# Kernel tuning notes

Measured on AMD Instinct MI355X. Metric: run time of the kernel, lower is better.

Reference implementation:

```python
import jax, jax.numpy as jnp
import numpy as np


def setup_inputs() -> dict:
    key = jax.random.key(0)
    ks = jax.random.split(key, 14)
    B, Ld, Lq, D = 64, 512, 128, 512
    d_node = jax.random.normal(ks[0], (B, Ld, D), jnp.float32)
    q_node = jax.random.normal(ks[1], (B, Lq, D), jnp.float32)
    qq_graph = jax.random.randint(ks[2], (B, Lq, Lq), 0, 2, jnp.int32)
    dq_graph = jax.random.randint(ks[3], (B, Ld, Lq), 0, 2, jnp.int32)
    dd_graph = jax.random.randint(ks[4], (B, Ld, Ld), 0, 2, jnp.int32)
    qd_graph = jax.random.randint(ks[5], (B, Lq, Ld), 0, 2, jnp.int32)
    s = 0.02
    W_nw = jax.random.normal(ks[6], (1, D), jnp.float32) * s
    b_nw = jnp.zeros((1,), jnp.float32)
    W_self = jax.random.normal(ks[7], (D, D), jnp.float32) * s
    b_self = jnp.zeros((D,), jnp.float32)
    W_dd = jax.random.normal(ks[8], (D, D), jnp.float32) * s
    W_qq = jax.random.normal(ks[9], (D, D), jnp.float32) * s
    W_dq = jax.random.normal(ks[10], (D, D), jnp.float32) * s
    W_qd = jax.random.normal(ks[11], (D, D), jnp.float32) * s
    return {"d_node": d_node, "q_node": q_node, "qq_graph": qq_graph,
            "dq_graph": dq_graph, "dd_graph": dd_graph, "qd_graph": qd_graph,
            "W_nw": W_nw, "b_nw": b_nw, "W_self": W_self, "b_self": b_self,
            "W_dd": W_dd, "W_qq": W_qq, "W_dq": W_dq, "W_qd": W_qd,
            "iteration_steps": 2}


def reference(d_node, q_node, qq_graph, dq_graph, dd_graph, qd_graph,
              W_nw, b_nw, W_self, b_self, W_dd, W_qq, W_dq, W_qd,
              iteration_steps):
    dd = dd_graph.astype(jnp.float32)
    dq = dq_graph.astype(jnp.float32)
    qq = qq_graph.astype(jnp.float32)
    qd = qd_graph.astype(jnp.float32)

    # neighbor counts, clamped to 1 where a node has no neighbors
    d_nb = dd.sum(-1) + dq.sum(-1)              # [B, Ld]
    d_nb = jnp.where(d_nb >= 1.0, d_nb, 1.0)
    q_nb = qq.sum(-1) + qd.sum(-1)              # [B, Lq]
    q_nb = jnp.where(q_nb >= 1.0, q_nb, 1.0)

    all_d_w, all_q_w = [], []
    for _ in range(iteration_steps):
        d_w = jax.nn.sigmoid(jnp.einsum('bld,od->blo', d_node, W_nw) + b_nw)[..., 0]  # [B, Ld]
        q_w = jax.nn.sigmoid(jnp.einsum('bld,od->blo', q_node, W_nw) + b_nw)[..., 0]  # [B, Lq]
        all_d_w.append(d_w)
        all_q_w.append(q_w)

        self_d = jnp.einsum('bld,od->blo', d_node, W_self) + b_self
        self_q = jnp.einsum('bld,od->blo', q_node, W_self) + b_self
        dd_info = jnp.einsum('bld,od->blo', d_node, W_dd)
        qd_info = jnp.einsum('bld,od->blo', d_node, W_qd)
        qq_info = jnp.einsum('bld,od->blo', q_node, W_qq)
        dq_info = jnp.einsum('bld,od->blo', q_node, W_dq)

        # masked weights: graph is 0/1, so replace_masked_values(., graph, 0) == graph * weight
        dd_msg = jnp.einsum('bij,bjd->bid', dd * d_w[:, None, :], dd_info)  # [B,Ld,D]
        qd_msg = jnp.einsum('bij,bjd->bid', qd * d_w[:, None, :], qd_info)  # [B,Lq,D]
        qq_msg = jnp.einsum('bij,bjd->bid', qq * q_w[:, None, :], qq_info)  # [B,Lq,D]
        dq_msg = jnp.einsum('bij,bjd->bid', dq * q_w[:, None, :], dq_info)  # [B,Ld,D]

        agg_q = (qq_msg + qd_msg) / q_nb[..., None]
        agg_d = (dd_msg + dq_msg) / d_nb[..., None]
        d_node = jax.nn.relu(self_d + agg_d)
        q_node = jax.nn.relu(self_q + agg_q)

    all_d_w = jnp.stack(all_d_w, axis=1)  # [B, steps, Ld]
    all_q_w = jnp.stack(all_q_w, axis=1)  # [B, steps, Lq]
    return (d_node, q_node, all_d_w, all_q_w)
```

## Files before the change

kernel.cpp:

```cpp
#include <hip/hip_runtime.h>
#include <cstdint>
#include <cstddef>

typedef _Float16 h16;
typedef __attribute__((ext_vector_type(8))) _Float16 h16x8;
typedef __attribute__((ext_vector_type(4))) _Float16 h16x4;
typedef __attribute__((ext_vector_type(4))) float f32x4;

constexpr int B_ = 64, LD = 512, LQ = 128, DIM = 512, STEPS = 2;
constexpr int MD = B_ * LD;
constexpr int MQ = B_ * LQ;
constexpr int KST = LD + LQ;
constexpr int KAGG = KST + DIM;

#define ASYNC16(gp, lp)                                                          \
  __builtin_amdgcn_global_load_lds(                                              \
      (const __attribute__((address_space(1))) unsigned int*)(gp),               \
      (__attribute__((address_space(3))) unsigned int*)(lp), 16, 0, 0)

struct Src {
  const h16* p0; int s0; long bstr0;
  const h16* p1; int s1; long bstr1;
  int ksplit;
};

template <int WM, class Epi>
__device__ __forceinline__ void gemm_body(int b, long tileM, long tileN,
                                          Src sa, Src sb, int K,
                                          const Epi& epi, h16* lds) {
  constexpr int BM = WM * 32;
  constexpr int AS = BM / 64;
  constexpr int AE = BM * 32;
  constexpr int BUFE = AE + 4096;

  const int tid = threadIdx.x;
  const int lane = tid & 63;
  const int wv = tid >> 6;
  const int wi = wv >> 1, wj = wv & 1;
  const int quad = lane >> 4, l16 = lane & 15;

  const int r = tid >> 2;
  const int es = (r ^ (r >> 2)) & 3;
  const int kq = (tid & 3) ^ es;

  const h16* pa[2][AS];
  const h16* pb[2][2];
#pragma unroll
  for (int s = 0; s < AS; s++) {
    pa[0][s] = sa.p0 + (size_t)b * sa.bstr0 + (tileM + r + 64 * s) * (long)sa.s0 + kq * 8;
    pa[1][s] = sa.p1 + (size_t)b * sa.bstr1 + (tileM + r + 64 * s) * (long)sa.s1 + kq * 8 - sa.ksplit;
  }
#pragma unroll
  for (int s = 0; s < 2; s++) {
    pb[0][s] = sb.p0 + (size_t)b * sb.bstr0 + (tileN + r + 64 * s) * (long)sb.s0 + kq * 8;
    pb[1][s] = sb.p1 + (size_t)b * sb.bstr1 + (tileN + r + 64 * s) * (long)sb.s1 + kq * 8 - sb.ksplit;
  }

  const int ef = (l16 ^ (l16 >> 2)) & 3;
  int offA[WM], offB[4];
#pragma unroll
  for (int i = 0; i < WM; i++) {
    const int row = wi * WM * 16 + i * 16 + l16;
    offA[i] = (row * 4 + (quad ^ ef)) * 8;
  }
#pragma unroll
  for (int j = 0; j < 4; j++) {
    const int row = wj * 64 + j * 16 + l16;
    offB[j] = AE + (row * 4 + (quad ^ ef)) * 8;
  }

  f32x4 acc[WM][4] = {};
  const int T = K >> 5;

  auto dmaTile = [&](int t, int off) {
    const int k0 = t * 32;
    h16* base = lds + off + tid * 8;
    const int sel = (k0 >= sa.ksplit);
#pragma unroll
    for (int s = 0; s < AS; s++) ASYNC16(pa[sel][s] + k0, base + s * 2048);
    const int selb = (k0 >= sb.ksplit);
#pragma unroll
    for (int s = 0; s < 2; s++) ASYNC16(pb[selb][s] + k0, base + AE + s * 2048);
  };
  auto mfmaStep = [&](int off) {
    h16x8 af[WM], bf[4];
#pragma unroll
    for (int i = 0; i < WM; i++) af[i] = *(const h16x8*)(lds + off + offA[i]);
#pragma unroll
    for (int j = 0; j < 4; j++) bf[j] = *(const h16x8*)(lds + off + offB[j]);
#pragma unroll
    for (int i = 0; i < WM; i++)
#pragma unroll
      for (int j = 0; j < 4; j++)
        acc[i][j] = __builtin_amdgcn_mfma_f32_16x16x32_f16(af[i], bf[j], acc[i][j], 0, 0, 0);
  };

  dmaTile(0, 0);
  dmaTile(1, BUFE);

  int co = 0;
  int no = 2 * BUFE;
  for (int t = 0; t < T - 1; ++t) {
    if constexpr (WM == 8) asm volatile("s_waitcnt vmcnt(6)" ::: "memory");
    else                   asm volatile("s_waitcnt vmcnt(4)" ::: "memory");
    __builtin_amdgcn_s_barrier();
    asm volatile("" ::: "memory");
    __builtin_amdgcn_sched_barrier(0);
    if (t + 2 < T) dmaTile(t + 2, no);
    mfmaStep(co);
    co = (co == 2 * BUFE) ? 0 : co + BUFE;
    no = (no == 2 * BUFE) ? 0 : no + BUFE;
  }
  asm volatile("s_waitcnt vmcnt(0)" ::: "memory");
  __builtin_amdgcn_s_barrier();
  asm volatile("" ::: "memory");
  __builtin_amdgcn_sched_barrier(0);
  mfmaStep(co);

#pragma unroll
  for (int i = 0; i < WM; i++) {
#pragma unroll
    for (int j = 0; j < 4; j++) {
      const int gm0 = (int)tileM + wi * WM * 16 + i * 16 + quad * 4;
      const int gn  = (int)tileN + wj * 64 + j * 16 + l16;
#pragma unroll
      for (int rr = 0; rr < 4; rr++) epi(b, gm0 + rr, gn, acc[i][j][rr]);
    }
  }
}

struct EpiDense {
  const float* w;
  h16* stackA;
  h16* stackB;
  int lnShift;
  int offA, offB;
  __device__ void operator()(int, int gm, int gn, float v) const {
    const int b = gn >> lnShift, l = gn & ((1 << lnShift) - 1);
    const h16 sv = (h16)(w[gn] * v);
    if (gm < 512)
      stackA[((size_t)b * 512 + gm) * 640 + offA + l] = sv;
    else
      stackB[((size_t)b * 512 + (gm - 512)) * 640 + offB + l] = sv;
  }
};
struct EpiAgg {
  const float* bias;
  float* out;
  h16* nodeNext;
  int rowsPerB;
  __device__ void operator()(int b, int gm, int gn, float v) const {
    const size_t row = (size_t)b * rowsPerB + gm;
    const float val = fmaxf(v + bias[gn], 0.f);
    if (out) out[row * 512 + gn] = val;
    if (nodeNext) nodeNext[row * 512 + gn] = (h16)val;
  }
};

__global__ __launch_bounds__(256, 2) void k_dense(Src saD, Src sbD, EpiDense epiD,
                                                  Src saQ, Src sbQ, EpiDense epiQ) {
  __shared__ __align__(16) h16 lds[3 * (256 * 32 + 128 * 32)];
  const int g = blockIdx.x;
  const int x = g / 320;
  const int yy = g % 320;
  if (yy < 256)
    gemm_body<8>(0, (long)x * 256, (long)yy * 128, saD, sbD, 512, epiD, lds);
  else
    gemm_body<8>(0, (long)x * 256, (long)(yy - 256) * 128, saQ, sbQ, 512, epiQ, lds);
}

__global__ __launch_bounds__(256, 2) void k_agg(Src saD, Src sbD, EpiAgg epiD,
                                                Src saQ, Src sbQ, EpiAgg epiQ) {
  __shared__ __align__(16) h16 lds[3 * (256 * 32 + 128 * 32)];
  const int g = blockIdx.x;
  const int b = g & 63;
  const int inner = g >> 6;
  if (inner >= 4) {
    const int i2 = inner - 4;
    gemm_body<8>(b, (long)(i2 >> 2) * 256, (long)(i2 & 3) * 128, saD, sbD, KAGG, epiD, lds);
  } else {
    gemm_body<4>(b, 0L, (long)inner * 128, saQ, sbQ, KAGG, epiQ, lds);
  }
}

__global__ __launch_bounds__(256) void k_convert(const float* __restrict__ dn,
                                                 const float* __restrict__ qn,
                                                 h16* __restrict__ dnb,
                                                 h16* __restrict__ qnb) {
  const size_t i4 = ((size_t)blockIdx.x * 256 + threadIdx.x) * 4;
  constexpr size_t TD = (size_t)MD * DIM;
  const float* src; h16* dst; size_t idx;
  if (i4 < TD) { src = dn; dst = dnb; idx = i4; }
  else         { src = qn; dst = qnb; idx = i4 - TD; }
  const float4 v = *(const float4*)&src[idx];
  h16x4 o; o.x = (h16)v.x; o.y = (h16)v.y; o.z = (h16)v.z; o.w = (h16)v.w;
  *(h16x4*)&dst[idx] = o;
}

__global__ __launch_bounds__(256) void k_wcat(const float* __restrict__ Wself,
                                              const float* __restrict__ Wdd,
                                              const float* __restrict__ Wqd,
                                              const float* __restrict__ Wqq,
                                              const float* __restrict__ Wdq,
                                              h16* __restrict__ catD,
                                              h16* __restrict__ catQ) {
  const int i = blockIdx.x * 256 + threadIdx.x;
  float vD, vQ;
  if (i < 512 * 512)       { vD = Wself[i];            vQ = vD; }
  else if (i < 1024 * 512) { vD = Wdd[i - 512 * 512];  vQ = Wqq[i - 512 * 512]; }
  else                     { vD = Wqd[i - 1024 * 512]; vQ = Wdq[i - 1024 * 512]; }
  catD[i] = (h16)vD; catQ[i] = (h16)vQ;
}

__global__ __launch_bounds__(256) void k_maskD(const int* __restrict__ dd,
                                               const int* __restrict__ dq,
                                               h16* __restrict__ maskD) {
  const int row = blockIdx.x * 4 + (threadIdx.x >> 6);
  const int lane = threadIdx.x & 63;
  const int* pdd = dd + (size_t)row * 512;
  const int* pdq = dq + (size_t)row * 128;
  h16* pm = maskD + (size_t)row * 640;
  float vals[10];
  float s = 0.f;
#pragma unroll
  for (int t = 0; t < 10; t++) {
    const int j = lane + t * 64;
    const float v = (float)((j < 512) ? pdd[j] : pdq[j - 512]);
    vals[t] = v; s += v;
  }
  for (int m = 32; m; m >>= 1) s += __shfl_xor(s, m);
  const float inv = 1.f / fmaxf(s, 1.f);
#pragma unroll
  for (int t = 0; t < 10; t++) pm[lane + t * 64] = (h16)(vals[t] * inv);
}

__global__ __launch_bounds__(256) void k_maskQ(const int* __restrict__ qq,
                                               const int* __restrict__ qd,
                                               h16* __restrict__ maskQ) {
  const int row = blockIdx.x * 4 + (threadIdx.x >> 6);
  const int lane = threadIdx.x & 63;
  const int* pqq = qq + (size_t)row * 128;
  const int* pqd = qd + (size_t)row * 512;
  h16* pm = maskQ + (size_t)row * 640;
  float vals[10];
  float s = 0.f;
#pragma unroll
  for (int t = 0; t < 10; t++) {
    const int j = lane + t * 64;
    const float v = (float)((j < 128) ? pqq[j] : pqd[j - 128]);
    vals[t] = v; s += v;
  }
  for (int m = 32; m; m >>= 1) s += __shfl_xor(s, m);
  const float inv = 1.f / fmaxf(s, 1.f);
#pragma unroll
  for (int t = 0; t < 10; t++) pm[lane + t * 64] = (h16)(vals[t] * inv);
}

__global__ __launch_bounds__(256) void k_w(const h16* __restrict__ dnb,
                                           const h16* __restrict__ qnb,
                                           const float* __restrict__ Wnw,
                                           const float* __restrict__ bnw,
                                           float* __restrict__ d_w,
                                           float* __restrict__ q_w,
                                           float* __restrict__ adw,
                                           float* __restrict__ aqw, int it) {
  const int row = blockIdx.x * 4 + (threadIdx.x >> 6);
  const int lane = threadIdx.x & 63;
  const bool isD = row < MD;
  const h16* node = isD ? dnb + (size_t)row * 512 : qnb + (size_t)(row - MD) * 512;
  const h16x8 v = *(const h16x8*)&node[lane * 8];
  const float4 w0 = *(const float4*)&Wnw[lane * 8];
  const float4 w1 = *(const float4*)&Wnw[lane * 8 + 4];
  float s = (float)v[0] * w0.x + (float)v[1] * w0.y + (float)v[2] * w0.z +
            (float)v[3] * w0.w + (float)v[4] * w1.x + (float)v[5] * w1.y +
            (float)v[6] * w1.z + (float)v[7] * w1.w;
  for (int m = 32; m; m >>= 1) s += __shfl_xor(s, m);
  if (lane == 0) {
    const float w = 1.f / (1.f + expf(-(s + bnw[0])));
    if (isD) {
      d_w[row] = w;
      adw[((size_t)(row >> 9) * STEPS + it) * 512 + (row & 511)] = w;
    } else {
      const int rq = row - MD;
      q_w[rq] = w;
      aqw[((size_t)(rq >> 7) * STEPS + it) * 128 + (rq & 127)] = w;
    }
  }
}

extern "C" void kernel_launch(void* const* d_in, const int* in_sizes, int n_in,
                              void* d_out, int out_size, void* d_ws, size_t ws_size,
                              hipStream_t stream) {
  (void)in_sizes; (void)n_in; (void)out_size; (void)ws_size;

  const float* d_node = (const float*)d_in[0];
  const float* q_node = (const float*)d_in[1];
  const int*   qq     = (const int*)d_in[2];
  const int*   dq     = (const int*)d_in[3];
  const int*   dd     = (const int*)d_in[4];
  const int*   qd     = (const int*)d_in[5];
  const float* W_nw   = (const float*)d_in[6];
  const float* b_nw   = (const float*)d_in[7];
  const float* W_self = (const float*)d_in[8];
  const float* b_self = (const float*)d_in[9];
  const float* W_dd   = (const float*)d_in[10];
  const float* W_qq   = (const float*)d_in[11];
  const float* W_dq   = (const float*)d_in[12];
  const float* W_qd   = (const float*)d_in[13];

  float* outd = (float*)d_out;
  float* outq = outd + (size_t)MD * DIM;
  float* adw  = outq + (size_t)MQ * DIM;
  float* aqw  = adw + (size_t)B_ * STEPS * LD;

  char* p = (char*)d_ws;
  auto alloc = [&](size_t bytes) { char* r = p; p += (bytes + 255) & ~(size_t)255; return r; };
  h16* dnode[2], *qnode[2];
  dnode[0] = (h16*)alloc((size_t)MD * DIM * 2);
  dnode[1] = (h16*)alloc((size_t)MD * DIM * 2);
  qnode[0] = (h16*)alloc((size_t)MQ * DIM * 2);
  qnode[1] = (h16*)alloc((size_t)MQ * DIM * 2);
  h16* catD    = (h16*)alloc((size_t)1536 * 512 * 2);
  h16* catQ    = (h16*)alloc((size_t)1536 * 512 * 2);
  h16* maskD   = (h16*)alloc((size_t)B_ * LD * KST * 2);
  h16* maskQ   = (h16*)alloc((size_t)B_ * LQ * KST * 2);
  h16* stackDT = (h16*)alloc((size_t)B_ * 512 * KST * 2);
  h16* stackQT = (h16*)alloc((size_t)B_ * 512 * KST * 2);
  float* d_wb  = (float*)alloc((size_t)MD * 4);
  float* q_wb  = (float*)alloc((size_t)MQ * 4);

  k_convert<<<dim3((MD * DIM + MQ * DIM) / 4 / 256), 256, 0, stream>>>(d_node, q_node, dnode[0], qnode[0]);
  k_wcat<<<dim3(1536 * 512 / 256), 256, 0, stream>>>(W_self, W_dd, W_qd, W_qq, W_dq, catD, catQ);
  k_maskD<<<dim3(MD / 4), 256, 0, stream>>>(dd, dq, maskD);
  k_maskQ<<<dim3(MQ / 4), 256, 0, stream>>>(qq, qd, maskQ);

  for (int it = 0; it < STEPS; it++) {
    const bool last = (it == STEPS - 1);
    h16* ncur_d = dnode[it & 1];
    h16* nnext_d = dnode[(it & 1) ^ 1];
    h16* ncur_q = qnode[it & 1];
    h16* nnext_q = qnode[(it & 1) ^ 1];

    k_w<<<dim3((MD + MQ) / 4), 256, 0, stream>>>(ncur_d, ncur_q, W_nw, b_nw, d_wb, q_wb, adw, aqw, it);

    {
      Src saD{catD + 512 * 512, 512, 0, catD + 512 * 512, 512, 0, 512};
      Src sbD{ncur_d, 512, 0, ncur_d, 512, 0, 512};
      Src saQ{catQ + 512 * 512, 512, 0, catQ + 512 * 512, 512, 0, 512};
      Src sbQ{ncur_q, 512, 0, ncur_q, 512, 0, 512};
      k_dense<<<dim3(1280), 256, 0, stream>>>(
          saD, sbD, EpiDense{d_wb, stackDT, stackQT, 9, 0, 128},
          saQ, sbQ, EpiDense{q_wb, stackQT, stackDT, 7, 0, 512});
    }
    {
      Src saD{maskD, 640, (long)LD * KST, ncur_d, 512, (long)LD * DIM, KST};
      Src sbD{stackDT, 640, (long)512 * KST, catD, 512, 0, KST};
      Src saQ{maskQ, 640, (long)LQ * KST, ncur_q, 512, (long)LQ * DIM, KST};
      Src sbQ{stackQT, 640, (long)512 * KST, catQ, 512, 0, KST};
      k_agg<<<dim3(768), 256, 0, stream>>>(
          saD, sbD, EpiAgg{b_self, last ? outd : nullptr, last ? nullptr : nnext_d, 512},
          saQ, sbQ, EpiAgg{b_self, last ? outq : nullptr, last ? nullptr : nnext_q, 128});
    }
  }
}
```

Baseline: 568.5 us.

## Enlarge GEMM block tiles to 256x256 with eight-wave 512-thread blocks

The shared GEMM body is reworked so a block covers 256 rows by 256 columns using eight waves (two rows by four columns) instead of 256x128 with four waves. The dense and aggregation launches are halved in block count and use 512 threads. Each operand tile loaded from global memory now feeds more MFMA work, which is meant to cut global and L2 traffic per flop. The cost is much larger LDS use per block (about 96 KB), which likely allows only one block per CU. The Q path with BM=128 also leaves waves 4-7 recomputing the same tiles as waves 0-3, so half its compute is duplicated.

```diff
diff --git a/kernel.cpp b/kernel.cpp
--- a/kernel.cpp
+++ b/kernel.cpp
@@ -24,52 +24,56 @@
   int ksplit;
 };
 
-template <int WM, class Epi>
+template <int BM, class Epi>
 __device__ __forceinline__ void gemm_body(int b, long tileM, long tileN,
                                           Src sa, Src sb, int K,
                                           const Epi& epi, h16* lds) {
-  constexpr int BM = WM * 32;
-  constexpr int AS = BM / 64;
   constexpr int AE = BM * 32;
-  constexpr int BUFE = AE + 4096;
+  constexpr int BUFE = AE + 256 * 32;
+  constexpr int NA = BM / 128;
 
   const int tid = threadIdx.x;
   const int lane = tid & 63;
   const int wv = tid >> 6;
-  const int wi = wv >> 1, wj = wv & 1;
+  const int wr = (BM == 256) ? (wv >> 2) : 0;
+  const int wc = wv & 3;
   const int quad = lane >> 4, l16 = lane & 15;
 
-  const int r = tid >> 2;
+  const int u = tid & 255;
+  const int sb2 = tid >> 8;
+  const int r = u >> 2;
   const int es = (r ^ (r >> 2)) & 3;
-  const int kq = (tid & 3) ^ es;
-
-  const h16* pa[2][AS];
+  const int kq = (u & 3) ^ es;
+
+  const h16* pa[2][NA];
   const h16* pb[2][2];
 #pragma unroll
-  for (int s = 0; s < AS; s++) {
-    pa[0][s] = sa.p0 + (size_t)b * sa.bstr0 + (tileM + r + 64 * s) * (long)sa.s0 + kq * 8;
-    pa[1][s] = sa.p1 + (size_t)b * sa.bstr1 + (tileM + r + 64 * s) * (long)sa.s1 + kq * 8 - sa.ksplit;
+  for (int s = 0; s < NA; s++) {
+    const long row = tileM + sb2 * 64 + r + 128 * s;
+    pa[0][s] = sa.p0 + (size_t)b * sa.bstr0 + row * (long)sa.s0 + kq * 8;
+    pa[1][s] = sa.p1 + (size_t)b * sa.bstr1 + row * (long)sa.s1 + kq * 8 - sa.ksplit;
   }
 #pragma unroll
   for (int s = 0; s < 2; s++) {
-    pb[0][s] = sb.p0 + (size_t)b * sb.bstr0 + (tileN + r + 64 * s) * (long)sb.s0 + kq * 8;
-    pb[1][s] = sb.p1 + (size_t)b * sb.bstr1 + (tileN + r + 64 * s) * (long)sb.s1 + kq * 8 - sb.ksplit;
+    const long row = tileN + sb2 * 64 + r + 128 * s;
+    pb[0][s] = sb.p0 + (size_t)b * sb.bstr0 + row * (long)sb.s0 + kq * 8;
+    pb[1][s] = sb.p1 + (size_t)b * sb.bstr1 + row * (long)sb.s1 + kq * 8 - sb.ksplit;
   }
 
   const int ef = (l16 ^ (l16 >> 2)) & 3;
-  int offA[WM], offB[4];
-#pragma unroll
-  for (int i = 0; i < WM; i++) {
-    const int row = wi * WM * 16 + i * 16 + l16;
+  int offA[8], offB[4];
+#pragma unroll
+  for (int i = 0; i < 8; i++) {
+    const int row = wr * 128 + i * 16 + l16;
     offA[i] = (row * 4 + (quad ^ ef)) * 8;
   }
 #pragma unroll
   for (int j = 0; j < 4; j++) {
-    const int row = wj * 64 + j * 16 + l16;
+    const int row = wc * 64 + j * 16 + l16;
     offB[j] = AE + (row * 4 + (quad ^ ef)) * 8;
   }
 
-  f32x4 acc[WM][4] = {};
+  f32x4 acc[8][4] = {};
   const int T = K >> 5;
 
   auto dmaTile = [&](int t, int off) {
@@ -77,19 +81,19 @@
     h16* base = lds + off + tid * 8;
     const int sel = (k0 >= sa.ksplit);
 #pragma unroll
-    for (int s = 0; s < AS; s++) ASYNC16(pa[sel][s] + k0, base + s * 2048);
+    for (int s = 0; s < NA; s++) ASYNC16(pa[sel][s] + k0, base + 4096 * s);
     const int selb = (k0 >= sb.ksplit);
 #pragma unroll
-    for (int s = 0; s < 2; s++) ASYNC16(pb[selb][s] + k0, base + AE + s * 2048);
+    for (int s = 0; s < 2; s++) ASYNC16(pb[selb][s] + k0, base + AE + 4096 * s);
   };
   auto mfmaStep = [&](int off) {
-    h16x8 af[WM], bf[4];
-#pragma unroll
-    for (int i = 0; i < WM; i++) af[i] = *(const h16x8*)(lds + off + offA[i]);
+    h16x8 af[8], bf[4];
+#pragma unroll
+    for (int i = 0; i < 8; i++) af[i] = *(const h16x8*)(lds + off + offA[i]);
 #pragma unroll
     for (int j = 0; j < 4; j++) bf[j] = *(const h16x8*)(lds + off + offB[j]);
 #pragma unroll
-    for (int i = 0; i < WM; i++)
+    for (int i = 0; i < 8; i++)
 #pragma unroll
       for (int j = 0; j < 4; j++)
         acc[i][j] = __builtin_amdgcn_mfma_f32_16x16x32_f16(af[i], bf[j], acc[i][j], 0, 0, 0);
@@ -101,8 +105,8 @@
   int co = 0;
   int no = 2 * BUFE;
   for (int t = 0; t < T - 1; ++t) {
-    if constexpr (WM == 8) asm volatile("s_waitcnt vmcnt(6)" ::: "memory");
-    else                   asm volatile("s_waitcnt vmcnt(4)" ::: "memory");
+    if constexpr (NA == 2) asm volatile("s_waitcnt vmcnt(4)" ::: "memory");
+    else                   asm volatile("s_waitcnt vmcnt(3)" ::: "memory");
     __builtin_amdgcn_s_barrier();
     asm volatile("" ::: "memory");
     __builtin_amdgcn_sched_barrier(0);
@@ -118,11 +122,11 @@
   mfmaStep(co);
 
 #pragma unroll
-  for (int i = 0; i < WM; i++) {
+  for (int i = 0; i < 8; i++) {
 #pragma unroll
     for (int j = 0; j < 4; j++) {
-      const int gm0 = (int)tileM + wi * WM * 16 + i * 16 + quad * 4;
-      const int gn  = (int)tileN + wj * 64 + j * 16 + l16;
+      const int gm0 = (int)tileM + wr * 128 + i * 16 + quad * 4;
+      const int gn  = (int)tileN + wc * 64 + j * 16 + l16;
 #pragma unroll
       for (int rr = 0; rr < 4; rr++) epi(b, gm0 + rr, gn, acc[i][j][rr]);
     }
@@ -157,29 +161,29 @@
   }
 };
 
-__global__ __launch_bounds__(256, 2) void k_dense(Src saD, Src sbD, EpiDense epiD,
+__global__ __launch_bounds__(512, 2) void k_dense(Src saD, Src sbD, EpiDense epiD,
                                                   Src saQ, Src sbQ, EpiDense epiQ) {
-  __shared__ __align__(16) h16 lds[3 * (256 * 32 + 128 * 32)];
+  __shared__ __align__(16) h16 lds[3 * (256 * 32 + 256 * 32)];
   const int g = blockIdx.x;
-  const int x = g / 320;
-  const int yy = g % 320;
-  if (yy < 256)
-    gemm_body<8>(0, (long)x * 256, (long)yy * 128, saD, sbD, 512, epiD, lds);
+  const int x = g / 160;
+  const int yy = g % 160;
+  if (yy < 128)
+    gemm_body<256>(0, (long)x * 256, (long)yy * 256, saD, sbD, 512, epiD, lds);
   else
-    gemm_body<8>(0, (long)x * 256, (long)(yy - 256) * 128, saQ, sbQ, 512, epiQ, lds);
-}
-
-__global__ __launch_bounds__(256, 2) void k_agg(Src saD, Src sbD, EpiAgg epiD,
+    gemm_body<256>(0, (long)x * 256, (long)(yy - 128) * 256, saQ, sbQ, 512, epiQ, lds);
+}
+
+__global__ __launch_bounds__(512, 2) void k_agg(Src saD, Src sbD, EpiAgg epiD,
                                                 Src saQ, Src sbQ, EpiAgg epiQ) {
-  __shared__ __align__(16) h16 lds[3 * (256 * 32 + 128 * 32)];
+  __shared__ __align__(16) h16 lds[3 * (256 * 32 + 256 * 32)];
   const int g = blockIdx.x;
   const int b = g & 63;
   const int inner = g >> 6;
-  if (inner >= 4) {
-    const int i2 = inner - 4;
-    gemm_body<8>(b, (long)(i2 >> 2) * 256, (long)(i2 & 3) * 128, saD, sbD, KAGG, epiD, lds);
+  if (inner >= 2) {
+    const int i2 = inner - 2;
+    gemm_body<256>(b, (long)(i2 >> 1) * 256, (long)(i2 & 1) * 256, saD, sbD, KAGG, epiD, lds);
   } else {
-    gemm_body<4>(b, 0L, (long)inner * 128, saQ, sbQ, KAGG, epiQ, lds);
+    gemm_body<128>(b, 0L, (long)inner * 256, saQ, sbQ, KAGG, epiQ, lds);
   }
 }
 
@@ -348,7 +352,7 @@
       Src sbD{ncur_d, 512, 0, ncur_d, 512, 0, 512};
       Src saQ{catQ + 512 * 512, 512, 0, catQ + 512 * 512, 512, 0, 512};
       Src sbQ{ncur_q, 512, 0, ncur_q, 512, 0, 512};
-      k_dense<<<dim3(1280), 256, 0, stream>>>(
+      k_dense<<<dim3(640), 512, 0, stream>>>(
           saD, sbD, EpiDense{d_wb, stackDT, stackQT, 9, 0, 128},
           saQ, sbQ, EpiDense{q_wb, stackQT, stackDT, 7, 0, 512});
     }
@@ -357,7 +361,7 @@
       Src sbD{stackDT, 640, (long)512 * KST, catD, 512, 0, KST};
       Src saQ{maskQ, 640, (long)LQ * KST, ncur_q, 512, (long)LQ * DIM, KST};
       Src sbQ{stackQT, 640, (long)512 * KST, catQ, 512, 0, KST};
-      k_agg<<<dim3(768), 256, 0, stream>>>(
+      k_agg<<<dim3(384), 512, 0, stream>>>(
           saD, sbD, EpiAgg{b_self, last ? outd : nullptr, last ? nullptr : nnext_d, 512},
           saQ, sbQ, EpiAgg{b_self, last ? outq : nullptr, last ? nullptr : nnext_q, 128});
     }
```

After: 620.1 us. 9.1% more time.
